# Performance work log

Hardware: AMD Instinct MI355X
Metric: run time of the kernel (lower is better)

The kernel has to match this reference:

```python
import jax, jax.numpy as jnp
import numpy as np

N_NODES = 50000
N_EDGES = 800000


def setup_inputs() -> dict:
    key = jax.random.key(0)
    ks = jax.random.split(key, 8)
    x = jax.random.normal(ks[0], (N_NODES, 256), dtype=jnp.float32)
    edge_index = jax.random.randint(ks[1], (2, N_EDGES), 0, N_NODES, dtype=jnp.int64)
    edge_weight = jax.random.uniform(ks[2], (N_EDGES,), dtype=jnp.float32)
    # Glorot-style weights for the 3 GCNConv layers: 256->128->64->32
    def glorot(k, fan_in, fan_out):
        s = jnp.sqrt(6.0 / (fan_in + fan_out))
        return jax.random.uniform(k, (fan_in, fan_out), dtype=jnp.float32, minval=-s, maxval=s)
    return {
        "x": x,
        "edge_index": edge_index,
        "edge_weight": edge_weight,
        "W1": glorot(ks[3], 256, 128), "b1": jnp.zeros((128,), jnp.float32),
        "W2": glorot(ks[4], 128, 64),  "b2": jnp.zeros((64,), jnp.float32),
        "W3": glorot(ks[5], 64, 32),   "b3": jnp.zeros((32,), jnp.float32),
    }


def _gcn_forward(x, row, col, ew, params):
    """Stacked GCNConv+ReLU (PyG semantics: add self loops, symmetric norm)."""
    n = x.shape[0]
    loop = jnp.arange(n, dtype=row.dtype)
    row_f = jnp.concatenate([row, loop])            # [E+N] sources
    col_f = jnp.concatenate([col, loop])            # [E+N] targets
    ew_f = jnp.concatenate([ew, jnp.ones((n,), ew.dtype)])
    deg = jax.ops.segment_sum(ew_f, col_f, num_segments=n)
    dinv = jnp.where(deg > 0, jax.lax.rsqrt(deg), 0.0)
    norm = dinv[row_f] * ew_f * dinv[col_f]         # [E+N]
    for W, b in params:
        h = x @ W                                   # [N, d_out] linear first (PyG order)
        msg = h[row_f] * norm[:, None]              # [E+N, d_out] gather + scale
        agg = jax.ops.segment_sum(msg, col_f, num_segments=n)  # scatter-add
        x = jax.nn.relu(agg + b)                    # fused bias + ReLU
    return x


def reference(x, edge_index, edge_weight, W1, b1, W2, b2, W3, b3):
    row, col = edge_index[0], edge_index[1]
    params = [(W1, b1), (W2, b2), (W3, b3)]
    return _gcn_forward(x, row, col, edge_weight, params)
```

## Files before the change

### kernel.cpp

```cpp
#include <hip/hip_runtime.h>
#include <hip/hip_fp16.h>


#define D0 256
#define D1 128
#define D2 64
#define D3 32

#define FIX_SCALE 16777216.0f
#define FIX_INV   (1.0f / 16777216.0f)

typedef _Float16 half8 __attribute__((ext_vector_type(8)));
typedef float floatx4 __attribute__((ext_vector_type(4)));

__global__ __launch_bounds__(256) void prep_kernel(
        const int* __restrict__ ei, const float* __restrict__ ew,
        unsigned long long* __restrict__ pk, int* __restrict__ rank, int E,
        const float* __restrict__ x, _Float16* __restrict__ x16, int xElems,
        const float* __restrict__ W1, _Float16* __restrict__ Wt1,
        const float* __restrict__ W2, _Float16* __restrict__ Wt2,
        const float* __restrict__ W3, _Float16* __restrict__ Wt3,
        int EB, int XB) {
    const int b = blockIdx.x;
    const int tid = threadIdx.x;
    if (b < EB) {
        int e = b * 256 + tid;
        if (e < E) {
            int c = ei[E + e];
            unsigned int wfix = (unsigned int)(ew[e] * FIX_SCALE + 0.5f);
            unsigned long long old =
                atomicAdd(&pk[c], (1ULL << 32) | (unsigned long long)wfix);
            rank[e] = (int)(old >> 32);
        }
    } else if (b < EB + XB) {
        int i = ((b - EB) * 256 + tid) * 8;
        if (i < xElems) {
            float4 f0 = *(const float4*)&x[i];
            float4 f1 = *(const float4*)&x[i + 4];
            half8 v;
            v[0] = (_Float16)f0.x; v[1] = (_Float16)f0.y;
            v[2] = (_Float16)f0.z; v[3] = (_Float16)f0.w;
            v[4] = (_Float16)f1.x; v[5] = (_Float16)f1.y;
            v[6] = (_Float16)f1.z; v[7] = (_Float16)f1.w;
            *(half8*)&x16[i] = v;
        }
    } else {
        int idx = (b - EB - XB) * 256 + tid;
        if (idx < D0 * D1) {
            int k = idx / D1, n = idx % D1;
            Wt1[n * D0 + k] = (_Float16)W1[idx];
        } else if (idx < D0 * D1 + D1 * D2) {
            int j = idx - D0 * D1;
            int k = j / D2, n = j % D2;
            Wt2[n * D1 + k] = (_Float16)W2[j];
        } else if (idx < D0 * D1 + D1 * D2 + D2 * D3) {
            int j = idx - D0 * D1 - D1 * D2;
            int k = j / D3, n = j % D3;
            Wt3[n * D2 + k] = (_Float16)W3[j];
        }
    }
}

__global__ __launch_bounds__(256) void scan_reduce(const unsigned long long* __restrict__ pk,
                                                   float* __restrict__ dinv,
                                                   int* __restrict__ cnt,
                                                   int* __restrict__ blockSum, int N) {
    __shared__ int s[256];
    const int t = threadIdx.x;
    const int i = blockIdx.x * 256 + t;
    int v = 0;
    if (i < N) {
        unsigned long long p = pk[i];
        float d = (float)(unsigned int)(p & 0xffffffffULL) * FIX_INV + 1.0f;
        dinv[i] = rsqrtf(d);
        v = (int)(p >> 32);
        cnt[i] = v;
    }
    s[t] = v;
    __syncthreads();
#pragma unroll
    for (int off = 128; off > 0; off >>= 1) {
        if (t < off) s[t] += s[t + off];
        __syncthreads();
    }
    if (t == 0) blockSum[blockIdx.x] = s[0];
}

__global__ __launch_bounds__(256) void scan_apply(const int* __restrict__ cnt,
                                                  const int* __restrict__ blockSum,
                                                  int* __restrict__ row_ptr, int N, int B) {
    __shared__ int bs[256];
    __shared__ int s[256];
    const int t = threadIdx.x;
    bs[t] = (t < B) ? blockSum[t] : 0;
    __syncthreads();
#pragma unroll
    for (int off = 1; off < 256; off <<= 1) {
        int u = (t >= off) ? bs[t - off] : 0;
        __syncthreads();
        bs[t] += u;
        __syncthreads();
    }
    const int myOff = (blockIdx.x > 0) ? bs[blockIdx.x - 1] : 0;
    const int i = blockIdx.x * 256 + t;
    const int v = (i < N) ? cnt[i] : 0;
    s[t] = v;
    __syncthreads();
#pragma unroll
    for (int off = 1; off < 256; off <<= 1) {
        int u = (t >= off) ? s[t - off] : 0;
        __syncthreads();
        s[t] += u;
        __syncthreads();
    }
    if (i < N) row_ptr[i] = s[t] - v + myOff;
    if (blockIdx.x == 0 && t == 0) row_ptr[N] = bs[B - 1];
}

__global__ void fill_kernel(const int* __restrict__ ei, const float* __restrict__ ew,
                            const float* __restrict__ dinv,
                            const int* __restrict__ row_ptr, const int* __restrict__ rank,
                            int2* __restrict__ pairs, int E) {
    int e = blockIdx.x * blockDim.x + threadIdx.x;
    if (e < E) {
        int r = ei[e];
        int c = ei[E + e];
        float w = dinv[r] * ew[e] * dinv[c];
        pairs[row_ptr[c] + rank[e]] = make_int2(r, __float_as_int(w));
    }
}

template <int K, int BN>
__global__ __launch_bounds__(256) void mfma_gemm(const _Float16* __restrict__ X,
                                                 const _Float16* __restrict__ Wt,
                                                 _Float16* __restrict__ H, int N) {
    constexpr int NC = K / 32;
    constexpr int CG = BN / 32;
    const int w = blockIdx.x * 4 + (threadIdx.x >> 6);
    const int lane = threadIdx.x & 63;
    const int quad = lane >> 4;
    const int m = lane & 15;
    const int cg = w & (CG - 1);
    const int nslab = N >> 4;
    const int stride = (gridDim.x * 4) / CG;
    int slab = w / CG;
    if (slab >= nslab) return;
    const int n0 = cg * 32;

    half8 b0[NC], b1[NC];
#pragma unroll
    for (int c = 0; c < NC; ++c) {
        b0[c] = *(const half8*)&Wt[(size_t)(n0 + m) * K + c * 32 + quad * 8];
        b1[c] = *(const half8*)&Wt[(size_t)(n0 + 16 + m) * K + c * 32 + quad * 8];
    }

    half8 a[NC];
#pragma unroll
    for (int c = 0; c < NC; ++c)
        a[c] = *(const half8*)&X[(size_t)(slab * 16 + m) * K + c * 32 + quad * 8];

    while (true) {
        const int next = slab + stride;
        half8 an[NC];
        if (next < nslab) {
#pragma unroll
            for (int c = 0; c < NC; ++c)
                an[c] = *(const half8*)&X[(size_t)(next * 16 + m) * K + c * 32 + quad * 8];
        }

        floatx4 acc0 = (floatx4){0.f, 0.f, 0.f, 0.f};
        floatx4 acc1 = (floatx4){0.f, 0.f, 0.f, 0.f};
#pragma unroll
        for (int c = 0; c < NC; ++c) {
            acc0 = __builtin_amdgcn_mfma_f32_16x16x32_f16(a[c], b0[c], acc0, 0, 0, 0);
            acc1 = __builtin_amdgcn_mfma_f32_16x16x32_f16(a[c], b1[c], acc1, 0, 0, 0);
        }

        const int r0 = slab * 16 + quad * 4;
#pragma unroll
        for (int r = 0; r < 4; ++r) {
            H[(size_t)(r0 + r) * BN + n0 + m]      = (_Float16)acc0[r];
            H[(size_t)(r0 + r) * BN + n0 + 16 + m] = (_Float16)acc1[r];
        }

        if (next >= nslab) break;
        slab = next;
#pragma unroll
        for (int c = 0; c < NC; ++c) a[c] = an[c];
    }
}

template <int D, typename OUT>
__global__ __launch_bounds__(256) void agg_kernel(const _Float16* __restrict__ H,
                                                  const int* __restrict__ row_ptr,
                                                  const int2* __restrict__ pairs,
                                                  const float* __restrict__ dinv,
                                                  const float* __restrict__ bias,
                                                  OUT* __restrict__ out, int N) {
    constexpr int TPN = D / 8;
    constexpr int NPB = 256 / TPN;
    const int tid = threadIdx.x;
    const int g = tid / TPN;
    const int lane = tid % TPN;
    const int node = blockIdx.x * NPB + g;
    if (node >= N) return;

    const int beg = row_ptr[node];
    const int end = row_ptr[node + 1];
    float acc[8];
#pragma unroll
    for (int j = 0; j < 8; ++j) acc[j] = 0.0f;

    if (end > beg) {
        const int last = end - 1;
        int2 p0 = pairs[beg];
        int2 p1 = pairs[min(beg + 1, last)];
        int2 p2 = pairs[min(beg + 2, last)];
        half8 u0 = *(const half8*)&H[(size_t)p0.x * D + lane * 8];
        half8 u1 = *(const half8*)&H[(size_t)p1.x * D + lane * 8];
        for (int k = beg; k < end; ++k) {
            int2 p3 = pairs[min(k + 3, last)];
            half8 u2 = *(const half8*)&H[(size_t)p2.x * D + lane * 8];
            float w = __int_as_float(p0.y);
#pragma unroll
            for (int j = 0; j < 8; ++j) acc[j] = fmaf(w, (float)u0[j], acc[j]);
            p0 = p1; p1 = p2; p2 = p3;
            u0 = u1; u1 = u2;
        }
    }
    float di = dinv[node];
    float d2 = di * di;
    {
        half8 u = *(const half8*)&H[(size_t)node * D + lane * 8];
#pragma unroll
        for (int j = 0; j < 8; ++j) acc[j] = fmaf(d2, (float)u[j], acc[j]);
    }
    float b[8];
    *(float4*)&b[0] = *(const float4*)&bias[lane * 8];
    *(float4*)&b[4] = *(const float4*)&bias[lane * 8 + 4];
#pragma unroll
    for (int j = 0; j < 8; ++j) acc[j] = fmaxf(acc[j] + b[j], 0.f);

    if constexpr (sizeof(OUT) == 2) {
        half8 o;
#pragma unroll
        for (int j = 0; j < 8; ++j) o[j] = (_Float16)acc[j];
        *(half8*)&out[(size_t)node * D + lane * 8] = o;
    } else {
        float* dst = (float*)&out[(size_t)node * D + lane * 8];
        *(float4*)&dst[0] = make_float4(acc[0], acc[1], acc[2], acc[3]);
        *(float4*)&dst[4] = make_float4(acc[4], acc[5], acc[6], acc[7]);
    }
}

extern "C" void kernel_launch(void* const* d_in, const int* in_sizes, int n_in,
                              void* d_out, int out_size, void* d_ws, size_t ws_size,
                              hipStream_t stream) {
    const float* x   = (const float*)d_in[0];
    const int* ei    = (const int*)d_in[1];
    const float* ew  = (const float*)d_in[2];
    const float* W1  = (const float*)d_in[3];
    const float* b1  = (const float*)d_in[4];
    const float* W2  = (const float*)d_in[5];
    const float* b2  = (const float*)d_in[6];
    const float* W3  = (const float*)d_in[7];
    const float* b3  = (const float*)d_in[8];
    float* out = (float*)d_out;

    const int N = in_sizes[0] / D0;
    const int E = in_sizes[2];
    (void)n_in; (void)out_size; (void)ws_size;

    char* ws = (char*)d_ws;
    size_t off = 0;
    auto carve = [&](size_t bytes) -> void* {
        void* p = (void*)(ws + off);
        off += (bytes + 255) & ~(size_t)255;
        return p;
    };
    unsigned long long* pk = (unsigned long long*)carve((size_t)N * 8);
    float* dinv    = (float*)carve((size_t)N * 4);
    int*   cnt     = (int*)carve((size_t)N * 4);
    int*   row_ptr = (int*)carve((size_t)(N + 1) * 4);
    int*   rank    = (int*)carve((size_t)E * 4);
    int*   bsum    = (int*)carve(256 * 4);
    int2*  pairs   = (int2*)carve((size_t)E * 8);
    _Float16* Wt1  = (_Float16*)carve((size_t)D0 * D1 * 2);
    _Float16* Wt2  = (_Float16*)carve((size_t)D1 * D2 * 2);
    _Float16* Wt3  = (_Float16*)carve((size_t)D2 * D3 * 2);
    _Float16* x16  = (_Float16*)carve((size_t)N * D0 * 2);
    _Float16* bufH = (_Float16*)carve((size_t)N * D1 * 2);
    _Float16* bufO = (_Float16*)carve((size_t)N * D1 * 2);

    _Float16* h1   = bufH;
    _Float16* out1 = bufO;
    _Float16* h2   = bufH;
    _Float16* out2 = bufO;
    _Float16* h3   = bufH;

    const int eb = (E + 255) / 256;
    const int xElems = N * D0;
    const int xb = (xElems / 8 + 255) / 256;
    const int wElems = D0 * D1 + D1 * D2 + D2 * D3;
    const int wb = (wElems + 255) / 256;
    const int scanB = (N + 255) / 256;
    const int gB = 768;

    hipMemsetAsync(pk, 0, (size_t)N * 8, stream);
    prep_kernel<<<eb + xb + wb, 256, 0, stream>>>(
        ei, ew, pk, rank, E, x, x16, xElems,
        W1, Wt1, W2, Wt2, W3, Wt3, eb, xb);

    scan_reduce<<<scanB, 256, 0, stream>>>(pk, dinv, cnt, bsum, N);
    scan_apply<<<scanB, 256, 0, stream>>>(cnt, bsum, row_ptr, N, scanB);
    fill_kernel<<<eb, 256, 0, stream>>>(ei, ew, dinv, row_ptr, rank, pairs, E);

    mfma_gemm<D0, D1><<<gB, 256, 0, stream>>>(x16, Wt1, h1, N);
    agg_kernel<D1, _Float16><<<(N + 15) / 16, 256, 0, stream>>>(h1, row_ptr, pairs, dinv, b1, out1, N);

    mfma_gemm<D1, D2><<<gB, 256, 0, stream>>>(out1, Wt2, h2, N);
    agg_kernel<D2, _Float16><<<(N + 31) / 32, 256, 0, stream>>>(h2, row_ptr, pairs, dinv, b2, out2, N);

    mfma_gemm<D2, D3><<<gB, 256, 0, stream>>>(out2, Wt3, h3, N);
    agg_kernel<D3, float><<<(N + 63) / 64, 256, 0, stream>>>(h3, row_ptr, pairs, dinv, b3, out, N);
}
```

Baseline: 269.0 us.

## Fuse fp32-to-fp16 conversion into GEMM loads and merge layer-1 GEMM with degree histogram

Removes the separate x→fp16 and weight-transpose prep passes. The GEMM now converts fp32 inputs and weights on load. The first-layer GEMM runs in the same launch as the edge-degree atomic histogram, so the two independent pieces of work overlap and one launch is saved. This avoids writing and re-reading the 25 MB fp16 copy of x. In exchange, each wave loads weights with strided scalar fp32 reads, and GEMM1 reads twice as many bytes for x.

Result: faster. 260.9 us (-3.0%).

```diff
diff --git a/kernel.cpp b/kernel.cpp
--- a/kernel.cpp
+++ b/kernel.cpp
@@ -13,18 +13,97 @@
 typedef _Float16 half8 __attribute__((ext_vector_type(8)));
 typedef float floatx4 __attribute__((ext_vector_type(4)));
 
-__global__ __launch_bounds__(256) void prep_kernel(
+template <typename SRC>
+__device__ __forceinline__ half8 loadA(const SRC* __restrict__ p) {
+    if constexpr (sizeof(SRC) == 4) {
+        float4 f0 = *(const float4*)p;
+        float4 f1 = *(const float4*)(p + 4);
+        half8 v;
+        v[0] = (_Float16)f0.x; v[1] = (_Float16)f0.y;
+        v[2] = (_Float16)f0.z; v[3] = (_Float16)f0.w;
+        v[4] = (_Float16)f1.x; v[5] = (_Float16)f1.y;
+        v[6] = (_Float16)f1.z; v[7] = (_Float16)f1.w;
+        return v;
+    } else {
+        return *(const half8*)p;
+    }
+}
+
+template <int K, int BN, typename SRC>
+__device__ __forceinline__ void gemm_work(const SRC* __restrict__ X,
+                                          const float* __restrict__ W,
+                                          _Float16* __restrict__ H, int N,
+                                          int w, int totalWaves) {
+    constexpr int NC = K / 32;
+    constexpr int CG = BN / 32;
+    const int lane = threadIdx.x & 63;
+    const int quad = lane >> 4;
+    const int m = lane & 15;
+    const int cg = w & (CG - 1);
+    const int nslab = N >> 4;
+    const int stride = totalWaves / CG;
+    int slab = w / CG;
+    if (slab >= nslab) return;
+    const int n0 = cg * 32;
+
+    half8 b0[NC], b1[NC];
+#pragma unroll
+    for (int c = 0; c < NC; ++c) {
+#pragma unroll
+        for (int j = 0; j < 8; ++j) {
+            int k = c * 32 + quad * 8 + j;
+            b0[c][j] = (_Float16)W[(size_t)k * BN + n0 + m];
+            b1[c][j] = (_Float16)W[(size_t)k * BN + n0 + 16 + m];
+        }
+    }
+
+    half8 a[NC];
+#pragma unroll
+    for (int c = 0; c < NC; ++c)
+        a[c] = loadA(&X[(size_t)(slab * 16 + m) * K + c * 32 + quad * 8]);
+
+    while (true) {
+        const int next = slab + stride;
+        half8 an[NC];
+        if (next < nslab) {
+#pragma unroll
+            for (int c = 0; c < NC; ++c)
+                an[c] = loadA(&X[(size_t)(next * 16 + m) * K + c * 32 + quad * 8]);
+        }
+
+        floatx4 acc0 = (floatx4){0.f, 0.f, 0.f, 0.f};
+        floatx4 acc1 = (floatx4){0.f, 0.f, 0.f, 0.f};
+#pragma unroll
+        for (int c = 0; c < NC; ++c) {
+            acc0 = __builtin_amdgcn_mfma_f32_16x16x32_f16(a[c], b0[c], acc0, 0, 0, 0);
+            acc1 = __builtin_amdgcn_mfma_f32_16x16x32_f16(a[c], b1[c], acc1, 0, 0, 0);
+        }
+
+        const int r0 = slab * 16 + quad * 4;
+#pragma unroll
+        for (int r = 0; r < 4; ++r) {
+            H[(size_t)(r0 + r) * BN + n0 + m]      = (_Float16)acc0[r];
+            H[(size_t)(r0 + r) * BN + n0 + 16 + m] = (_Float16)acc1[r];
+        }
+
+        if (next >= nslab) break;
+        slab = next;
+#pragma unroll
+        for (int c = 0; c < NC; ++c) a[c] = an[c];
+    }
+}
+
+__global__ __launch_bounds__(256) void hist_gemm1_kernel(
+        const float* __restrict__ x, const float* __restrict__ W1,
+        _Float16* __restrict__ h1, int N,
         const int* __restrict__ ei, const float* __restrict__ ew,
         unsigned long long* __restrict__ pk, int* __restrict__ rank, int E,
-        const float* __restrict__ x, _Float16* __restrict__ x16, int xElems,
-        const float* __restrict__ W1, _Float16* __restrict__ Wt1,
-        const float* __restrict__ W2, _Float16* __restrict__ Wt2,
-        const float* __restrict__ W3, _Float16* __restrict__ Wt3,
-        int EB, int XB) {
+        int gB) {
     const int b = blockIdx.x;
-    const int tid = threadIdx.x;
-    if (b < EB) {
-        int e = b * 256 + tid;
+    if (b < gB) {
+        gemm_work<D0, D1, float>(x, W1, h1, N, b * 4 + (threadIdx.x >> 6), gB * 4);
+    } else {
+        int e = (b - gB) * 256 + threadIdx.x;
         if (e < E) {
             int c = ei[E + e];
             unsigned int wfix = (unsigned int)(ew[e] * FIX_SCALE + 0.5f);
@@ -32,33 +111,14 @@
                 atomicAdd(&pk[c], (1ULL << 32) | (unsigned long long)wfix);
             rank[e] = (int)(old >> 32);
         }
-    } else if (b < EB + XB) {
-        int i = ((b - EB) * 256 + tid) * 8;
-        if (i < xElems) {
-            float4 f0 = *(const float4*)&x[i];
-            float4 f1 = *(const float4*)&x[i + 4];
-            half8 v;
-            v[0] = (_Float16)f0.x; v[1] = (_Float16)f0.y;
-            v[2] = (_Float16)f0.z; v[3] = (_Float16)f0.w;
-            v[4] = (_Float16)f1.x; v[5] = (_Float16)f1.y;
-            v[6] = (_Float16)f1.z; v[7] = (_Float16)f1.w;
-            *(half8*)&x16[i] = v;
-        }
-    } else {
-        int idx = (b - EB - XB) * 256 + tid;
-        if (idx < D0 * D1) {
-            int k = idx / D1, n = idx % D1;
-            Wt1[n * D0 + k] = (_Float16)W1[idx];
-        } else if (idx < D0 * D1 + D1 * D2) {
-            int j = idx - D0 * D1;
-            int k = j / D2, n = j % D2;
-            Wt2[n * D1 + k] = (_Float16)W2[j];
-        } else if (idx < D0 * D1 + D1 * D2 + D2 * D3) {
-            int j = idx - D0 * D1 - D1 * D2;
-            int k = j / D3, n = j % D3;
-            Wt3[n * D2 + k] = (_Float16)W3[j];
-        }
-    }
+    }
+}
+
+template <int K, int BN, typename SRC>
+__global__ __launch_bounds__(256) void mfma_gemm(const SRC* __restrict__ X,
+                                                 const float* __restrict__ W,
+                                                 _Float16* __restrict__ H, int N) {
+    gemm_work<K, BN, SRC>(X, W, H, N, blockIdx.x * 4 + (threadIdx.x >> 6), gridDim.x * 4);
 }
 
 __global__ __launch_bounds__(256) void scan_reduce(const unsigned long long* __restrict__ pk,
@@ -130,66 +190,6 @@
     }
 }
 
-template <int K, int BN>
-__global__ __launch_bounds__(256) void mfma_gemm(const _Float16* __restrict__ X,
-                                                 const _Float16* __restrict__ Wt,
-                                                 _Float16* __restrict__ H, int N) {
-    constexpr int NC = K / 32;
-    constexpr int CG = BN / 32;
-    const int w = blockIdx.x * 4 + (threadIdx.x >> 6);
-    const int lane = threadIdx.x & 63;
-    const int quad = lane >> 4;
-    const int m = lane & 15;
-    const int cg = w & (CG - 1);
-    const int nslab = N >> 4;
-    const int stride = (gridDim.x * 4) / CG;
-    int slab = w / CG;
-    if (slab >= nslab) return;
-    const int n0 = cg * 32;
-
-    half8 b0[NC], b1[NC];
-#pragma unroll
-    for (int c = 0; c < NC; ++c) {
-        b0[c] = *(const half8*)&Wt[(size_t)(n0 + m) * K + c * 32 + quad * 8];
-        b1[c] = *(const half8*)&Wt[(size_t)(n0 + 16 + m) * K + c * 32 + quad * 8];
-    }
-
-    half8 a[NC];
-#pragma unroll
-    for (int c = 0; c < NC; ++c)
-        a[c] = *(const half8*)&X[(size_t)(slab * 16 + m) * K + c * 32 + quad * 8];
-
-    while (true) {
-        const int next = slab + stride;
-        half8 an[NC];
-        if (next < nslab) {
-#pragma unroll
-            for (int c = 0; c < NC; ++c)
-                an[c] = *(const half8*)&X[(size_t)(next * 16 + m) * K + c * 32 + quad * 8];
-        }
-
-        floatx4 acc0 = (floatx4){0.f, 0.f, 0.f, 0.f};
-        floatx4 acc1 = (floatx4){0.f, 0.f, 0.f, 0.f};
-#pragma unroll
-        for (int c = 0; c < NC; ++c) {
-            acc0 = __builtin_amdgcn_mfma_f32_16x16x32_f16(a[c], b0[c], acc0, 0, 0, 0);
-            acc1 = __builtin_amdgcn_mfma_f32_16x16x32_f16(a[c], b1[c], acc1, 0, 0, 0);
-        }
-
-        const int r0 = slab * 16 + quad * 4;
-#pragma unroll
-        for (int r = 0; r < 4; ++r) {
-            H[(size_t)(r0 + r) * BN + n0 + m]      = (_Float16)acc0[r];
-            H[(size_t)(r0 + r) * BN + n0 + 16 + m] = (_Float16)acc1[r];
-        }
-
-        if (next >= nslab) break;
-        slab = next;
-#pragma unroll
-        for (int c = 0; c < NC; ++c) a[c] = an[c];
-    }
-}
-
 template <int D, typename OUT>
 __global__ __launch_bounds__(256) void agg_kernel(const _Float16* __restrict__ H,
                                                   const int* __restrict__ row_ptr,
@@ -285,10 +285,6 @@
     int*   rank    = (int*)carve((size_t)E * 4);
     int*   bsum    = (int*)carve(256 * 4);
     int2*  pairs   = (int2*)carve((size_t)E * 8);
-    _Float16* Wt1  = (_Float16*)carve((size_t)D0 * D1 * 2);
-    _Float16* Wt2  = (_Float16*)carve((size_t)D1 * D2 * 2);
-    _Float16* Wt3  = (_Float16*)carve((size_t)D2 * D3 * 2);
-    _Float16* x16  = (_Float16*)carve((size_t)N * D0 * 2);
     _Float16* bufH = (_Float16*)carve((size_t)N * D1 * 2);
     _Float16* bufO = (_Float16*)carve((size_t)N * D1 * 2);
 
@@ -299,28 +295,22 @@
     _Float16* h3   = bufH;
 
     const int eb = (E + 255) / 256;
-    const int xElems = N * D0;
-    const int xb = (xElems / 8 + 255) / 256;
-    const int wElems = D0 * D1 + D1 * D2 + D2 * D3;
-    const int wb = (wElems + 255) / 256;
     const int scanB = (N + 255) / 256;
     const int gB = 768;
 
     hipMemsetAsync(pk, 0, (size_t)N * 8, stream);
-    prep_kernel<<<eb + xb + wb, 256, 0, stream>>>(
-        ei, ew, pk, rank, E, x, x16, xElems,
-        W1, Wt1, W2, Wt2, W3, Wt3, eb, xb);
+    hist_gemm1_kernel<<<gB + eb, 256, 0, stream>>>(
+        x, W1, h1, N, ei, ew, pk, rank, E, gB);
 
     scan_reduce<<<scanB, 256, 0, stream>>>(pk, dinv, cnt, bsum, N);
     scan_apply<<<scanB, 256, 0, stream>>>(cnt, bsum, row_ptr, N, scanB);
     fill_kernel<<<eb, 256, 0, stream>>>(ei, ew, dinv, row_ptr, rank, pairs, E);
 
-    mfma_gemm<D0, D1><<<gB, 256, 0, stream>>>(x16, Wt1, h1, N);
     agg_kernel<D1, _Float16><<<(N + 15) / 16, 256, 0, stream>>>(h1, row_ptr, pairs, dinv, b1, out1, N);
 
-    mfma_gemm<D1, D2><<<gB, 256, 0, stream>>>(out1, Wt2, h2, N);
+    mfma_gemm<D1, D2, _Float16><<<gB, 256, 0, stream>>>(out1, W2, h2, N);
     agg_kernel<D2, _Float16><<<(N + 31) / 32, 256, 0, stream>>>(h2, row_ptr, pairs, dinv, b2, out2, N);
 
-    mfma_gemm<D2, D3><<<gB, 256, 0, stream>>>(out2, Wt3, h3, N);
+    mfma_gemm<D2, D3, _Float16><<<gB, 256, 0, stream>>>(out2, W3, h3, N);
     agg_kernel<D3, float><<<(N + 63) / 64, 256, 0, stream>>>(h3, row_ptr, pairs, dinv, b3, out, N);
 }
```
